# Kernel tuning notes

Hardware: AMD Instinct MI355X
Metric: run time of the kernel (lower is better)

Reference implementation:

```python
import jax, jax.numpy as jnp
import numpy as np
from jax import lax

RADIUS = 0.1
K = 32
STRIDE = 4
BN_EPS = 1e-5


def fps(xyz, m):
    """Furthest point sampling. xyz: (B,N,3) -> idx (B,m) int32. Starts at index 0."""
    B, N, _ = xyz.shape

    def body(carry, _):
        dists, last_idx = carry  # (B,N), (B,)
        last = jnp.take_along_axis(xyz, last_idx[:, None, None], axis=1)  # (B,1,3)
        d = jnp.sum((xyz - last) ** 2, axis=-1)  # (B,N)
        dists = jnp.minimum(dists, d)
        nxt = jnp.argmax(dists, axis=1).astype(jnp.int32)
        return (dists, nxt), nxt

    init_idx = jnp.zeros((B,), jnp.int32)
    init_d = jnp.full((B, N), 1e10, xyz.dtype)
    _, idxs = lax.scan(body, (init_d, init_idx), None, length=m - 1)  # (m-1,B)
    return jnp.concatenate([init_idx[None, :], idxs], axis=0).T  # (B,m)


def ball_query(new_xyz, xyz, radius, k):
    """First-k-in-index-order points within radius (pointnet2 semantics).
    new_xyz: (B,M,3), xyz: (B,N,3) -> idx (B,M,k). Slots past the count are
    filled with the first valid index."""
    B, N, _ = xyz.shape
    d2 = jnp.sum((new_xyz[:, :, None, :] - xyz[:, None, :, :]) ** 2, axis=-1)  # (B,M,N)
    mask = d2 < radius * radius
    order = jnp.where(mask, jnp.arange(N, dtype=jnp.int32), N)
    first_k = jnp.sort(order, axis=-1)[..., :k]  # (B,M,k)
    valid = first_k < N
    first = first_k[..., :1]  # centroid itself is always within radius
    return jnp.where(valid, first_k, first)


def setup_inputs() -> dict:
    key = jax.random.key(0)
    ks = jax.random.split(key, 8)
    B, N, C0, C1, C2 = 2, 8192, 64, 128, 256
    xyz = jax.random.uniform(ks[0], (B, N, 3), jnp.float32)
    x = jax.random.normal(ks[1], (B, C0, N), jnp.float32)
    W1 = jax.random.normal(ks[2], (C1, 3 + C0), jnp.float32) * 0.05
    b1 = jnp.zeros((C1,), jnp.float32)
    W2 = jax.random.normal(ks[3], (C2, C1), jnp.float32) * 0.05
    b2 = jnp.zeros((C2,), jnp.float32)
    gamma = jnp.ones((C2,), jnp.float32)
    beta = jnp.zeros((C2,), jnp.float32)
    return dict(xyz=xyz, x=x, W1=W1, b1=b1, W2=W2, b2=b2, gamma=gamma, beta=beta)


def reference(xyz, x, W1, b1, W2, b2, gamma, beta):
    B, N, _ = xyz.shape
    M = N // STRIDE
    fidx = fps(xyz, M)                                   # (B,M)
    b = jnp.arange(B)[:, None]
    new_xyz = xyz[b, fidx]                               # (B,M,3)
    idx = ball_query(new_xyz, xyz, RADIUS, K)            # (B,M,K)
    bi = jnp.arange(B)[:, None, None]
    rel = xyz[bi, idx] - new_xyz[:, :, None, :]          # (B,M,K,3) relative coords
    feats = jnp.transpose(x, (0, 2, 1))                  # (B,N,C0)
    group = jnp.concatenate([rel, feats[bi, idx]], axis=-1)  # (B,M,K,3+C0), xyz first
    # pointwise MLP (1x1 convs)
    h = jax.nn.relu(jnp.einsum('bmkc,oc->bmko', group, W1) + b1)
    h = jnp.einsum('bmkc,oc->bmko', h, W2) + b2          # (B,M,K,C2)
    p = jnp.max(h, axis=2)                               # (B,M,C2) max-pool over neighbors
    # BatchNorm1d, training-mode batch stats (biased variance)
    mean = jnp.mean(p, axis=(0, 1))
    var = jnp.var(p, axis=(0, 1))
    out = (p - mean) / jnp.sqrt(var + BN_EPS) * gamma + beta
    return new_xyz, jnp.transpose(out, (0, 2, 1))        # (B,M,3), (B,C2,M)
```

## Files before the change

kernel.cpp:

```cpp
#include <hip/hip_runtime.h>
#include <cstdint>
#include <cstddef>

#define B_   2
#define N_   8192
#define M_   2048
#define K_   32
#define C0_  64
#define C1_  128
#define C2_  256
#define CIN_ 67

__device__ __forceinline__ float sqdist_rn(float ax, float ay, float az,
                                           float bx, float by, float bz) {
  float dx = __fsub_rn(ax, bx);
  float dy = __fsub_rn(ay, by);
  float dz = __fsub_rn(az, bz);
  return __fadd_rn(__fadd_rn(__fmul_rn(dx, dx), __fmul_rn(dy, dy)),
                   __fmul_rn(dz, dz));
}

__device__ __forceinline__ int morton8(int ix, int iy, int iz) {
  int m = 0;
#pragma unroll
  for (int b = 0; b < 3; ++b) {
    m |= (((ix >> b) & 1) << (3 * b + 2)) | (((iy >> b) & 1) << (3 * b + 1)) |
         (((iz >> b) & 1) << (3 * b + 0));
  }
  return m;
}

__device__ __forceinline__ unsigned long long wave_max_u64_dpp(unsigned long long k) {
#define FPS_STEP(ctrl)                                                         \
  {                                                                            \
    int klo = (int)(unsigned)k, khi = (int)(unsigned)(k >> 32);                \
    int olo = __builtin_amdgcn_update_dpp(klo, klo, ctrl, 0xf, 0xf, false);    \
    int ohi = __builtin_amdgcn_update_dpp(khi, khi, ctrl, 0xf, 0xf, false);    \
    unsigned long long ok =                                                    \
        ((unsigned long long)(unsigned)ohi << 32) | (unsigned)olo;             \
    if (ok > k) k = ok;                                                        \
  }
  FPS_STEP(0x111)
  FPS_STEP(0x112)
  FPS_STEP(0x114)
  FPS_STEP(0x118)
  FPS_STEP(0x142)
  FPS_STEP(0x143)
#undef FPS_STEP
  return k;
}

__global__ __launch_bounds__(1024, 1) void fps_kernel(const float* __restrict__ xyz,
                                                      float* __restrict__ new_xyz) {
  const int b = blockIdx.x;
  const int t = threadIdx.x;
  const int lane = t & 63;
  const int w = t >> 6;
  const float* xb = xyz + (size_t)b * N_ * 3;

  __shared__ float4 spt[N_];
  __shared__ float snew3[M_ * 3];
  __shared__ unsigned long long sKey[16];
  __shared__ int hist[512];
  __shared__ int boff[512];
  __shared__ int wsum[8];

  if (t < 512) hist[t] = 0;
  __syncthreads();
#pragma unroll
  for (int rr = 0; rr < 8; ++rr) {
    int i = rr * 1024 + t;
    float X = xb[i * 3 + 0], Y = xb[i * 3 + 1], Z = xb[i * 3 + 2];
    int ix = min(7, max(0, (int)(X * 8.0f)));
    int iy = min(7, max(0, (int)(Y * 8.0f)));
    int iz = min(7, max(0, (int)(Z * 8.0f)));
    atomicAdd(&hist[morton8(ix, iy, iz)], 1);
  }
  __syncthreads();
  {
    int ov = (t < 512) ? hist[t] : 0;
    int v = ov;
#pragma unroll
    for (int off = 1; off < 64; off <<= 1) {
      int n = __shfl_up(v, off);
      if (lane >= off) v += n;
    }
    if (t < 512 && lane == 63) wsum[w] = v;
    __syncthreads();
    if (t == 0) {
      int acc = 0;
#pragma unroll
      for (int j = 0; j < 8; ++j) { int x0 = wsum[j]; wsum[j] = acc; acc += x0; }
    }
    __syncthreads();
    if (t < 512) boff[t] = v - ov + wsum[w];
  }
  __syncthreads();
#pragma unroll
  for (int rr = 0; rr < 8; ++rr) {
    int i = rr * 1024 + t;
    float X = xb[i * 3 + 0], Y = xb[i * 3 + 1], Z = xb[i * 3 + 2];
    int ix = min(7, max(0, (int)(X * 8.0f)));
    int iy = min(7, max(0, (int)(Y * 8.0f)));
    int iz = min(7, max(0, (int)(Z * 8.0f)));
    int pos = atomicAdd(&boff[morton8(ix, iy, iz)], 1);
    float4 v4; v4.x = X; v4.y = Y; v4.z = Z; v4.w = __int_as_float(i);
    spt[pos] = v4;
  }
  if (t == 0) {
    snew3[0] = xb[0]; snew3[1] = xb[1]; snew3[2] = xb[2];
  }
  __syncthreads();

  float px[8], py[8], pz[8], d[8];
  unsigned lowk[8];
#pragma unroll
  for (int k = 0; k < 8; ++k) {
    float4 v4 = spt[8 * t + k];
    px[k] = v4.x; py[k] = v4.y; pz[k] = v4.z;
    int pid = __float_as_int(v4.w);
    lowk[k] = ((unsigned)(8191 - pid) << 13) | (unsigned)(8 * t + k);
    d[k] = 1e10f;
  }
  float cx = 0.f, cy = 0.f, cz = 0.f;
#pragma unroll
  for (int k = 0; k < 8; ++k) { cx += px[k]; cy += py[k]; cz += pz[k]; }
  cx *= 0.125f; cy *= 0.125f; cz *= 0.125f;
  float r2m = 0.f;
#pragma unroll
  for (int k = 0; k < 8; ++k) {
    float dx = px[k] - cx, dy = py[k] - cy, dz = pz[k] - cz;
    r2m = fmaxf(r2m, dx * dx + dy * dy + dz * dz);
  }
  const float rad = sqrtf(r2m) * 1.00002f + 1e-12f;

  unsigned long long tkey = 0ull;
  float thrT = 3e38f;

  for (int it = 1; it < M_; ++it) {
    const float lx = snew3[it * 3 - 3];
    const float ly = snew3[it * 3 - 2];
    const float lz = snew3[it * 3 - 1];

    float ex = lx - cx, ey = ly - cy, ez = lz - cz;
    float dc2 = ex * ex + ey * ey + ez * ez;
    bool dirtyLane = dc2 <= thrT;
    if (__ballot(dirtyLane) != 0ull) {
      if (dirtyLane) {
        unsigned long long nk = 0ull;
#pragma unroll
        for (int k = 0; k < 8; ++k) {
          float dist = sqdist_rn(px[k], py[k], pz[k], lx, ly, lz);
          float dm = fminf(d[k], dist);
          d[k] = dm;
          unsigned long long key =
              ((unsigned long long)(unsigned)__float_as_int(dm) << 26) | lowk[k];
          nk = (key > nk) ? key : nk;
        }
        tkey = nk;
        float bd = __int_as_float((int)(unsigned)(tkey >> 26));
        float sr = sqrtf(bd * 1.0001f) + rad;
        thrT = sr * sr;
      }
      unsigned long long wk = wave_max_u64_dpp(tkey);
      if (lane == 63) sKey[w] = wk;
    }
    __syncthreads();
    if (w == 0) {
      unsigned long long key = sKey[lane & 15];
#define FPS_STEP2(ctrl)                                                        \
      {                                                                        \
        int klo = (int)(unsigned)key, khi = (int)(unsigned)(key >> 32);        \
        int olo = __builtin_amdgcn_update_dpp(klo, klo, ctrl, 0xf, 0xf, false);\
        int ohi = __builtin_amdgcn_update_dpp(khi, khi, ctrl, 0xf, 0xf, false);\
        unsigned long long okey =                                              \
            ((unsigned long long)(unsigned)ohi << 32) | (unsigned)olo;         \
        if (okey > key) key = okey;                                            \
      }
      FPS_STEP2(0x111)
      FPS_STEP2(0x112)
      FPS_STEP2(0x114)
      FPS_STEP2(0x118)
#undef FPS_STEP2
      int winPos = __builtin_amdgcn_readlane((int)(unsigned)key, 15) & 8191;
      float4 c = spt[winPos];
      if (lane == 0) {
        snew3[it * 3 + 0] = c.x;
        snew3[it * 3 + 1] = c.y;
        snew3[it * 3 + 2] = c.z;
      }
    }
    __syncthreads();
  }

  for (int i = t; i < M_ * 3; i += 1024) {
    new_xyz[(size_t)b * M_ * 3 + i] = snew3[i];
  }
}

__global__ __launch_bounds__(256) void mlp_kernel(const float* __restrict__ xyz,
                                                  const float* __restrict__ x,
                                                  const float* __restrict__ W1,
                                                  const float* __restrict__ b1,
                                                  const float* __restrict__ W2,
                                                  const float* __restrict__ b2,
                                                  const float* __restrict__ new_xyz,
                                                  float* __restrict__ outp) {
  __shared__ float sGRed[32 * 69];
  __shared__ float sU[128 * 69];
  __shared__ float sH1[32 * 132];
  __shared__ int sWIdx[4][K_];
  __shared__ int sWCnt[4];
  __shared__ int sIdx[K_];
  __shared__ float sQ[3];

  const int gm = blockIdx.x;
  const int b = gm >> 11;
  const int m = gm & 2047;
  const int t = threadIdx.x;
  const int lane = t & 63;
  const int w = t >> 6;
  const float* xb = xyz + (size_t)b * N_ * 3;

  if (t < 3) sQ[t] = new_xyz[(size_t)gm * 3 + t];
  __syncthreads();
  const float qx = sQ[0], qy = sQ[1], qz = sQ[2];
  const float R2 = (float)(0.1 * 0.1);

  {
    int cnt = 0;
    const int cbeg = w * 2048, cend = cbeg + 2048;
    for (int base = cbeg; base < cend; base += 64) {
      int p = base + lane;
      float d2 = sqdist_rn(qx, qy, qz, xb[p * 3 + 0], xb[p * 3 + 1], xb[p * 3 + 2]);
      bool valid = d2 < R2;
      unsigned long long mask = __ballot(valid);
      if (valid) {
        int pos = cnt + __popcll(mask & ((1ull << lane) - 1ull));
        if (pos < K_) sWIdx[w][pos] = p;
      }
      cnt += __popcll(mask);
      if (cnt >= K_) break;
    }
    if (lane == 0) sWCnt[w] = (cnt < K_) ? cnt : K_;
  }
  __syncthreads();
  if (t < K_) {
    int c0 = sWCnt[0], c1 = sWCnt[1], c2 = sWCnt[2], c3 = sWCnt[3];
    int s1 = c0 + c1, s2 = s1 + c2, s3 = s2 + c3;
    int j = t, idx;
    if (j < c0) idx = sWIdx[0][j];
    else if (j < s1) idx = sWIdx[1][j - c0];
    else if (j < s2) idx = sWIdx[2][j - s1];
    else if (j < s3) idx = sWIdx[3][j - s2];
    else {
      int fw = c0 ? 0 : (c1 ? 1 : (c2 ? 2 : 3));
      idx = (s3 > 0) ? sWIdx[fw][0] : 0;
    }
    sIdx[j] = idx;
  }
  __syncthreads();

  if (t < K_) {
    int id = sIdx[t];
    sGRed[t * 69 + 0] = xb[id * 3 + 0] - qx;
    sGRed[t * 69 + 1] = xb[id * 3 + 1] - qy;
    sGRed[t * 69 + 2] = xb[id * 3 + 2] - qz;
  }
  {
    int r = t & 31;
    int c0 = (t >> 5) * 8;
    int id = sIdx[r];
    const float* xf = x + ((size_t)b * C0_ + c0) * N_ + id;
#pragma unroll
    for (int j = 0; j < 8; ++j) sGRed[r * 69 + 3 + c0 + j] = xf[(size_t)j * N_];
  }
  for (int i = t; i < C1_ * CIN_; i += 256) {
    sU[(i / CIN_) * 69 + (i % CIN_)] = W1[i];
  }
  __syncthreads();

  const int ol = t & 31;
  const int rg = t >> 5;

  float acc[4][4] = {{0.f}};
  for (int c = 0; c < CIN_; ++c) {
    float g[4], wv[4];
#pragma unroll
    for (int i = 0; i < 4; ++i) g[i] = sGRed[(rg * 4 + i) * 69 + c];
#pragma unroll
    for (int j = 0; j < 4; ++j) wv[j] = sU[(ol + 32 * j) * 69 + c];
#pragma unroll
    for (int i = 0; i < 4; ++i)
#pragma unroll
      for (int j = 0; j < 4; ++j) acc[i][j] += g[i] * wv[j];
  }
#pragma unroll
  for (int j = 0; j < 4; ++j) {
    float bias = b1[ol + 32 * j];
#pragma unroll
    for (int i = 0; i < 4; ++i) {
      float v = acc[i][j] + bias;
      sH1[(rg * 4 + i) * 132 + ol + 32 * j] = fmaxf(v, 0.0f);
    }
  }

  float acc2[4][8] = {{0.f}};
  for (int ct = 0; ct < 4; ++ct) {
    __syncthreads();
    const float4* w4 = (const float4*)(W2 + (size_t)t * C1_ + ct * 32);
#pragma unroll
    for (int jj = 0; jj < 8; ++jj) {
      float4 v = w4[jj];
      sU[(jj * 4 + 0) * 256 + t] = v.x;
      sU[(jj * 4 + 1) * 256 + t] = v.y;
      sU[(jj * 4 + 2) * 256 + t] = v.z;
      sU[(jj * 4 + 3) * 256 + t] = v.w;
    }
    __syncthreads();
    for (int cc = 0; cc < 32; ++cc) {
      float h[4], wv[8];
#pragma unroll
      for (int i = 0; i < 4; ++i) h[i] = sH1[(rg * 4 + i) * 132 + ct * 32 + cc];
#pragma unroll
      for (int j = 0; j < 8; ++j) wv[j] = sU[cc * 256 + ol + 32 * j];
#pragma unroll
      for (int i = 0; i < 4; ++i)
#pragma unroll
        for (int j = 0; j < 8; ++j) acc2[i][j] += h[i] * wv[j];
    }
  }

  __syncthreads();
#pragma unroll
  for (int j = 0; j < 8; ++j) {
    float pm = acc2[0][j];
#pragma unroll
    for (int i = 1; i < 4; ++i) pm = fmaxf(pm, acc2[i][j]);
    sGRed[rg * 256 + ol + 32 * j] = pm;
  }
  __syncthreads();
  {
    int o = t;
    float v = sGRed[o];
#pragma unroll
    for (int g = 1; g < 8; ++g) v = fmaxf(v, sGRed[g * 256 + o]);
    v += b2[o];
    outp[((size_t)(b * C2_ + o)) * M_ + m] = v;
  }
}

__global__ __launch_bounds__(256) void bn_stats_kernel(const float* __restrict__ outp,
                                                       const float* __restrict__ gamma,
                                                       float* __restrict__ stats) {
  const int o = blockIdx.x;
  const int t = threadIdx.x;
  double s = 0.0, s2 = 0.0;
  for (int b = 0; b < B_; ++b) {
    const float* p = outp + ((size_t)(b * C2_ + o)) * M_;
    for (int i = t; i < M_; i += 256) {
      float v = p[i];
      s += (double)v;
      s2 += (double)v * (double)v;
    }
  }
#pragma unroll
  for (int off = 32; off > 0; off >>= 1) {
    s += __shfl_xor(s, off);
    s2 += __shfl_xor(s2, off);
  }
  __shared__ double aS[4], aS2[4];
  if ((t & 63) == 0) { aS[t >> 6] = s; aS2[t >> 6] = s2; }
  __syncthreads();
  if (t == 0) {
    double S = aS[0] + aS[1] + aS[2] + aS[3];
    double S2 = aS2[0] + aS2[1] + aS2[2] + aS2[3];
    double mean = S / (double)(B_ * M_);
    double var = S2 / (double)(B_ * M_) - mean * mean;
    float rstd = 1.0f / sqrtf((float)var + 1e-5f);
    stats[o] = (float)mean;
    stats[C2_ + o] = gamma[o] * rstd;
  }
}

__global__ __launch_bounds__(256) void bn_apply_kernel(float* __restrict__ outp,
                                                       const float* __restrict__ stats,
                                                       const float* __restrict__ beta) {
  const int i4 = blockIdx.x * 256 + threadIdx.x;
  const int ch = (i4 >> 9) & 255;
  const float mean = stats[ch];
  const float scale = stats[C2_ + ch];
  const float bt = beta[ch];
  float4 v = ((const float4*)outp)[i4];
  v.x = (v.x - mean) * scale + bt;
  v.y = (v.y - mean) * scale + bt;
  v.z = (v.z - mean) * scale + bt;
  v.w = (v.w - mean) * scale + bt;
  ((float4*)outp)[i4] = v;
}

extern "C" void kernel_launch(void* const* d_in, const int* in_sizes, int n_in,
                              void* d_out, int out_size, void* d_ws, size_t ws_size,
                              hipStream_t stream) {
  const float* xyz   = (const float*)d_in[0];
  const float* x     = (const float*)d_in[1];
  const float* W1    = (const float*)d_in[2];
  const float* b1    = (const float*)d_in[3];
  const float* W2    = (const float*)d_in[4];
  const float* b2    = (const float*)d_in[5];
  const float* gamma = (const float*)d_in[6];
  const float* beta  = (const float*)d_in[7];

  float* new_xyz = (float*)d_out;
  float* outp    = (float*)d_out + (size_t)B_ * M_ * 3;
  float* stats   = (float*)d_ws;

  fps_kernel<<<B_, 1024, 0, stream>>>(xyz, new_xyz);
  mlp_kernel<<<B_ * M_, 256, 0, stream>>>(xyz, x, W1, b1, W2, b2, new_xyz, outp);
  bn_stats_kernel<<<C2_, 256, 0, stream>>>(outp, gamma, stats);
  bn_apply_kernel<<<(B_ * C2_ * M_ / 4) / 256, 256, 0, stream>>>(outp, stats, beta);
}
```

Measured before the change: 2.779 ms.

## Remove second barrier in FPS loop via redundant per-wave final reduction

```diff
diff --git a/kernel.cpp b/kernel.cpp
--- a/kernel.cpp
+++ b/kernel.cpp
@@ -47,23 +47,27 @@
   FPS_STEP(0x142)
   FPS_STEP(0x143)
 #undef FPS_STEP
-  return k;
+  unsigned lo = (unsigned)__builtin_amdgcn_readlane((int)(unsigned)k, 63);
+  unsigned hi = (unsigned)__builtin_amdgcn_readlane((int)(unsigned)(k >> 32), 63);
+  return ((unsigned long long)hi << 32) | lo;
 }
 
 __global__ __launch_bounds__(1024, 1) void fps_kernel(const float* __restrict__ xyz,
                                                       float* __restrict__ new_xyz) {
+  __shared__ __align__(16) unsigned char ldsbuf[156416];
+  float4* spt   = (float4*)(ldsbuf);
+  float*  snew3 = (float*)(ldsbuf + 131072);
+  int*    hist  = (int*)(ldsbuf + 131072);
+  int*    boff  = (int*)(ldsbuf + 131072 + 2048);
+  int*    wsum  = (int*)(ldsbuf + 131072 + 4096);
+  unsigned long long* sKeyP = (unsigned long long*)(ldsbuf + 155648);
+  float4* sCrdP = (float4*)(ldsbuf + 155904);
+
   const int b = blockIdx.x;
   const int t = threadIdx.x;
   const int lane = t & 63;
   const int w = t >> 6;
   const float* xb = xyz + (size_t)b * N_ * 3;
-
-  __shared__ float4 spt[N_];
-  __shared__ float snew3[M_ * 3];
-  __shared__ unsigned long long sKey[16];
-  __shared__ int hist[512];
-  __shared__ int boff[512];
-  __shared__ int wsum[8];
 
   if (t < 512) hist[t] = 0;
   __syncthreads();
@@ -107,9 +111,6 @@
     float4 v4; v4.x = X; v4.y = Y; v4.z = Z; v4.w = __int_as_float(i);
     spt[pos] = v4;
   }
-  if (t == 0) {
-    snew3[0] = xb[0]; snew3[1] = xb[1]; snew3[2] = xb[2];
-  }
   __syncthreads();
 
   float px[8], py[8], pz[8], d[8];
@@ -119,7 +120,7 @@
     float4 v4 = spt[8 * t + k];
     px[k] = v4.x; py[k] = v4.y; pz[k] = v4.z;
     int pid = __float_as_int(v4.w);
-    lowk[k] = ((unsigned)(8191 - pid) << 13) | (unsigned)(8 * t + k);
+    lowk[k] = (unsigned)(8191 - pid) << 13;
     d[k] = 1e10f;
   }
   float cx = 0.f, cy = 0.f, cz = 0.f;
@@ -134,20 +135,23 @@
   }
   const float rad = sqrtf(r2m) * 1.00002f + 1e-12f;
 
-  unsigned long long tkey = 0ull;
+  unsigned long long tkey = 0ull, wk = 0ull;
   float thrT = 3e38f;
+  float bcx = px[0], bcy = py[0], bcz = pz[0];
+  float wcx = 0.f, wcy = 0.f, wcz = 0.f;
+
+  float lx = xb[0], ly = xb[1], lz = xb[2];
+  if (t == 0) { snew3[0] = lx; snew3[1] = ly; snew3[2] = lz; }
 
   for (int it = 1; it < M_; ++it) {
-    const float lx = snew3[it * 3 - 3];
-    const float ly = snew3[it * 3 - 2];
-    const float lz = snew3[it * 3 - 1];
-
+    const int wp = it & 1;
     float ex = lx - cx, ey = ly - cy, ez = lz - cz;
     float dc2 = ex * ex + ey * ey + ez * ez;
     bool dirtyLane = dc2 <= thrT;
     if (__ballot(dirtyLane) != 0ull) {
       if (dirtyLane) {
         unsigned long long nk = 0ull;
+        float nx = bcx, ny = bcy, nz = bcz;
 #pragma unroll
         for (int k = 0; k < 8; ++k) {
           float dist = sqdist_rn(px[k], py[k], pz[k], lx, ly, lz);
@@ -155,43 +159,69 @@
           d[k] = dm;
           unsigned long long key =
               ((unsigned long long)(unsigned)__float_as_int(dm) << 26) | lowk[k];
-          nk = (key > nk) ? key : nk;
+          bool take = key > nk;
+          nk = take ? key : nk;
+          nx = take ? px[k] : nx;
+          ny = take ? py[k] : ny;
+          nz = take ? pz[k] : nz;
         }
-        tkey = nk;
+        tkey = nk; bcx = nx; bcy = ny; bcz = nz;
         float bd = __int_as_float((int)(unsigned)(tkey >> 26));
         float sr = sqrtf(bd * 1.0001f) + rad;
         thrT = sr * sr;
       }
-      unsigned long long wk = wave_max_u64_dpp(tkey);
-      if (lane == 63) sKey[w] = wk;
+      unsigned long long wkn = wave_max_u64_dpp(tkey);
+      unsigned long long tied = __ballot(tkey == wkn);
+      int src = __ffsll((long long)tied) - 1;
+      wk = wkn;
+      wcx = __builtin_amdgcn_readlane(__float_as_int(bcx), src) == 0
+                ? __int_as_float(__builtin_amdgcn_readlane(__float_as_int(bcx), src))
+                : __int_as_float(__builtin_amdgcn_readlane(__float_as_int(bcx), src));
+      wcx = __int_as_float(__builtin_amdgcn_readlane(__float_as_int(bcx), src));
+      wcy = __int_as_float(__builtin_amdgcn_readlane(__float_as_int(bcy), src));
+      wcz = __int_as_float(__builtin_amdgcn_readlane(__float_as_int(bcz), src));
+    }
+    if (lane == 63) {
+      sKeyP[wp * 16 + w] = wk;
+      float4 c4; c4.x = wcx; c4.y = wcy; c4.z = wcz; c4.w = 0.f;
+      sCrdP[wp * 16 + w] = c4;
     }
     __syncthreads();
-    if (w == 0) {
-      unsigned long long key = sKey[lane & 15];
+    {
+      int sl = lane & 15;
+      unsigned long long korig = sKeyP[wp * 16 + sl];
+      float4 c4 = sCrdP[wp * 16 + sl];
+      unsigned long long kred = korig;
 #define FPS_STEP2(ctrl)                                                        \
       {                                                                        \
-        int klo = (int)(unsigned)key, khi = (int)(unsigned)(key >> 32);        \
+        int klo = (int)(unsigned)kred, khi = (int)(unsigned)(kred >> 32);      \
         int olo = __builtin_amdgcn_update_dpp(klo, klo, ctrl, 0xf, 0xf, false);\
         int ohi = __builtin_amdgcn_update_dpp(khi, khi, ctrl, 0xf, 0xf, false);\
         unsigned long long okey =                                              \
             ((unsigned long long)(unsigned)ohi << 32) | (unsigned)olo;         \
-        if (okey > key) key = okey;                                            \
+        if (okey > kred) kred = okey;                                          \
       }
       FPS_STEP2(0x111)
       FPS_STEP2(0x112)
       FPS_STEP2(0x114)
       FPS_STEP2(0x118)
 #undef FPS_STEP2
-      int winPos = __builtin_amdgcn_readlane((int)(unsigned)key, 15) & 8191;
-      float4 c = spt[winPos];
-      if (lane == 0) {
-        snew3[it * 3 + 0] = c.x;
-        snew3[it * 3 + 1] = c.y;
-        snew3[it * 3 + 2] = c.z;
-      }
-    }
-    __syncthreads();
-  }
+      unsigned mlo = (unsigned)__builtin_amdgcn_readlane((int)(unsigned)kred, 15);
+      unsigned mhi = (unsigned)__builtin_amdgcn_readlane((int)(unsigned)(kred >> 32), 15);
+      unsigned long long kmax = ((unsigned long long)mhi << 32) | mlo;
+      unsigned long long tied2 = __ballot(korig == kmax);
+      int src2 = __ffsll((long long)tied2) - 1;
+      lx = __int_as_float(__builtin_amdgcn_readlane(__float_as_int(c4.x), src2));
+      ly = __int_as_float(__builtin_amdgcn_readlane(__float_as_int(c4.y), src2));
+      lz = __int_as_float(__builtin_amdgcn_readlane(__float_as_int(c4.z), src2));
+    }
+    if (t == 0) {
+      snew3[it * 3 + 0] = lx;
+      snew3[it * 3 + 1] = ly;
+      snew3[it * 3 + 2] = lz;
+    }
+  }
+  __syncthreads();
 
   for (int i = t; i < M_ * 3; i += 1024) {
     new_xyz[(size_t)b * M_ * 3 + i] = snew3[i];
```

After: 3.415 ms. 22.9% more time.
